# Kernel tuning notes

Hardware: AMD Instinct MI355X
Metric: run time of the kernel (lower is better)

Reference implementation:

```python
import jax, jax.numpy as jnp
import numpy as np

# dims: batch, samples, agents, obs_dim, action_dim, hidden
B, S, N, D, A, H = 512, 64, 8, 64, 16, 256
IN_DIM = (D + A) * N  # 640


def mish(x):
    return x * jnp.tanh(jax.nn.softplus(x))


def setup_inputs() -> dict:
    key = jax.random.key(0)
    ks = jax.random.split(key, 9)
    u = lambda k, shape, fan_in: jax.random.uniform(
        k, shape, jnp.float32, -1.0 / np.sqrt(fan_in), 1.0 / np.sqrt(fan_in))
    return {
        "state": jax.random.normal(ks[0], (B, N, D), jnp.float32),
        "action": jax.random.normal(ks[1], (B, N, A), jnp.float32),
        "W1": u(ks[2], (IN_DIM, H), IN_DIM),
        "b1": u(ks[3], (H,), IN_DIM),
        "W2": u(ks[4], (H, H), H),
        "b2": u(ks[5], (H,), H),
        "W3": u(ks[6], (H, 1), H),
        "b3": u(ks[7], (1,), H),
        # random grand-coalition permutations of the N agents, per (batch, sample)
        "perm": jnp.argsort(jax.random.uniform(ks[8], (B, S, N)), axis=-1).astype(jnp.int32),
    }


def reference(state, action, W1, b1, W2, b2, W3, b3, perm):
    # subcoalition mask [B,S,N,N]: torch builds one-hot(perm) @ tril(ones),
    # i.e. mask[b,s,i,j] = 1 iff j <= perm[b,s,i]
    subcoal = (jnp.arange(N) <= perm[..., None]).astype(state.dtype)
    # gathered actions in coalition order [B,S,N,A]: act_g[b,s,j] = action[b, perm[b,s,j]]
    act_g = action[jnp.arange(B)[:, None, None], perm]
    # masked subcoalition actions [B,S,N,N,A] -> [B,S,N,N*A]
    act = (act_g[:, :, None, :, :] * subcoal[..., None]).reshape(B, S, N, N * A)
    # flattened global obs broadcast over (sample, agent) axes [B,S,N,N*D]
    obs = jnp.broadcast_to(state.reshape(B, 1, 1, N * D), (B, S, N, N * D))
    x = jnp.concatenate([obs, act], axis=-1)  # [B,S,N,IN_DIM]
    # per-agent loop in torch uses shared q1 weights -> single batched MLP
    h = mish(x @ W1 + b1)
    h = mish(h @ W2 + b2)
    q = h @ W3 + b3                   # [B,S,N,1]
    q1 = q.mean(axis=1).squeeze(-1)   # mean over samples -> [B,N]
    return (q1, q1)
```

## Files before the change

kernel.cpp:

```cpp
#include <hip/hip_runtime.h>
#include <hip/hip_bf16.h>

typedef unsigned short ushort_t;
typedef _Float16 half_t;
typedef __attribute__((ext_vector_type(2))) _Float16 half2_t;
typedef __attribute__((ext_vector_type(8))) _Float16 half8_t;
typedef __attribute__((ext_vector_type(2))) float fx2;
typedef __attribute__((ext_vector_type(4))) float floatx4;

#define LOG2E 1.4426950408889634f
#define LN2   0.6931471805599453f

__device__ __forceinline__ float exp2_(float x) {
#if __has_builtin(__builtin_amdgcn_exp2f)
    return __builtin_amdgcn_exp2f(x);
#else
    return exp2f(x);
#endif
}

__device__ __forceinline__ half2_t cvt_pk_f16(float a, float b) {
    auto r = __builtin_amdgcn_cvt_pkrtz(a, b);
    return __builtin_bit_cast(half2_t, r);
}

__device__ __forceinline__ fx2 mish2(fx2 t0) {
    fx2 one = {1.0f, 1.0f};
    fx2 m2  = {-2.0f, -2.0f};
    fx2 u   = {exp2_(t0.x), exp2_(t0.y)};
    fx2 s   = u + one;
    fx2 wv  = __builtin_elementwise_fma(s, s, one);
    fx2 rr  = {__builtin_amdgcn_rcpf(wv.x), __builtin_amdgcn_rcpf(wv.y)};
    fx2 v   = __builtin_elementwise_fma(rr, m2, one);
    return t0 * v;
}

__device__ __forceinline__ float dpp_sum16(float v) {
    int x = __float_as_int(v);
    v += __int_as_float(__builtin_amdgcn_update_dpp(0, x, 0xB1, 0xF, 0xF, true));
    x = __float_as_int(v);
    v += __int_as_float(__builtin_amdgcn_update_dpp(0, x, 0x4E, 0xF, 0xF, true));
    x = __float_as_int(v);
    v += __int_as_float(__builtin_amdgcn_update_dpp(0, x, 0x124, 0xF, 0xF, true));
    x = __float_as_int(v);
    v += __int_as_float(__builtin_amdgcn_update_dpp(0, x, 0x128, 0xF, 0xF, true));
    return v;
}

__global__ __launch_bounds__(256) void prep_kernel(
        const float* __restrict__ state,
        const float* __restrict__ action,
        const float* __restrict__ W1,
        const float* __restrict__ b1,
        const float* __restrict__ W2,
        float* __restrict__ obsW,
        half_t* __restrict__ actW,
        half_t* __restrict__ W2T,
        float* __restrict__ out) {
    int bid = blockIdx.x;
    int t = threadIdx.x;
    if (bid < 512) {
        int b = bid;
        const float* stp = state + (size_t)b * 512;
        const float* w1p = W1 + t;
        float a0 = 0.f, a1 = 0.f, a2 = 0.f, a3 = 0.f;
#pragma unroll 8
        for (int f = 0; f < 512; f += 4) {
            a0 = fmaf(stp[f + 0], w1p[(f + 0) * 256], a0);
            a1 = fmaf(stp[f + 1], w1p[(f + 1) * 256], a1);
            a2 = fmaf(stp[f + 2], w1p[(f + 2) * 256], a2);
            a3 = fmaf(stp[f + 3], w1p[(f + 3) * 256], a3);
        }
        obsW[b * 256 + t] = ((a0 + a1) + (a2 + a3) + b1[t]) * LOG2E;
    } else if (bid < 2560) {
        int idx = bid - 512;
        int j = idx & 7;
        int b0 = (idx >> 3) * 2;
        const float* W1a = W1 + (size_t)(512 + j * 16) * 256;
        float wv[16];
#pragma unroll
        for (int a = 0; a < 16; ++a) wv[a] = W1a[a * 256 + t];
#pragma unroll
        for (int bb = 0; bb < 2; ++bb) {
            int b = b0 + bb;
            const float* acp = action + (size_t)b * 128;
            float acc[8];
#pragma unroll
            for (int n = 0; n < 8; ++n) acc[n] = 0.f;
#pragma unroll
            for (int a = 0; a < 16; ++a) {
#pragma unroll
                for (int n = 0; n < 8; ++n)
                    acc[n] = fmaf(acp[n * 16 + a], wv[a], acc[n]);
            }
#pragma unroll
            for (int n = 0; n < 8; ++n)
                actW[(((size_t)b * 8 + n) * 8 + j) * 256 + t] = (half_t)(acc[n] * LOG2E);
        }
    } else {
        int blk = bid - 2560;
        if (blk < 16) {
            out[blk * 512 + t] = 0.0f;
            out[blk * 512 + 256 + t] = 0.0f;
        }
        int n = blk * 8 + (t >> 5);
        int klo = t & 31;
#pragma unroll
        for (int kk = 0; kk < 8; ++kk) {
            int k = kk * 32 + klo;
            W2T[n * 256 + k] = (half_t)W2[k * 256 + n];
        }
    }
}

#define CHUNK_US 528

__global__ __launch_bounds__(512, 4) void main_kernel(
        const float* __restrict__ obsW, const half_t* __restrict__ actW,
        const half_t* __restrict__ W2T, const int* __restrict__ perm,
        const float* __restrict__ b2,
        const float* __restrict__ W3, const float* __restrict__ b3,
        float* __restrict__ out) {
    __shared__ __align__(16) ushort_t h1[32 * CHUNK_US];
    __shared__ __align__(16) float obsb[256];
    __shared__ int perm_s[64];
    __shared__ float qpart[8][64];
    __shared__ float qv_s[64];

    int t = threadIdx.x;
    int bid = blockIdx.x;
    int b = (bid & 7) * 64 + ((bid >> 3) & 63);
    int sg = bid >> 9;
    int s0 = sg * 8;

    int w = t >> 6;
    int L = t & 63;
    int lo = L & 15;
    int q = L >> 4;

    if (t < 256) obsb[t] = obsW[b * 256 + t];
    else if (t < 320) perm_s[t - 256] = perm[((size_t)b * 64 + s0) * 8 + (t - 256)];

    const half_t* w2base = W2T + ((size_t)(w * 32 + lo)) * 256 + q * 8;
    half8_t bpre[4];
    bpre[0] = *reinterpret_cast<const half8_t*>(w2base + 0 * 16 * 256 + 0 * 32);
    bpre[1] = *reinterpret_cast<const half8_t*>(w2base + 1 * 16 * 256 + 0 * 32);
    bpre[2] = *reinterpret_cast<const half8_t*>(w2base + 0 * 16 * 256 + 1 * 32);
    bpre[3] = *reinterpret_cast<const half8_t*>(w2base + 1 * 16 * 256 + 1 * 32);

    __syncthreads();

    {
        int sl = w;
        int hg = L;
        int g = hg >> 1;
        int ks = g >> 2;
        int qq = g & 3;
        int half = hg & 1;
        const half_t* actg = actW + (size_t)b * 64 * 256 + hg * 4;
        uint2 av[8];
#pragma unroll
        for (int j = 0; j < 8; ++j) {
            int p = perm_s[sl * 8 + j];
            av[j] = *reinterpret_cast<const uint2*>(actg + (p * 8 + j) * 256);
        }
        float4 ob = *reinterpret_cast<const float4*>(obsb + hg * 4);
        fx2 r01 = {ob.x, ob.y};
        fx2 r23 = {ob.z, ob.w};
        ushort_t* dst0 = h1 + (qq * 16) * 8 + half * 4 + ks * CHUNK_US;
#pragma unroll
        for (int j = 0; j < 8; ++j) {
            half2_t a0 = __builtin_bit_cast(half2_t, av[j].x);
            half2_t a1 = __builtin_bit_cast(half2_t, av[j].y);
            r01 += (fx2){(float)a0.x, (float)a0.y};
            r23 += (fx2){(float)a1.x, (float)a1.y};
            fx2 h01 = mish2(r01);
            fx2 h23 = mish2(r23);
            half2_t p0 = cvt_pk_f16(h01.x, h01.y);
            half2_t p1 = cvt_pk_f16(h23.x, h23.y);
            int row = sl * 8 + j;
            int mt = row >> 4, lr = row & 15;
            uint2 pk = make_uint2(__builtin_bit_cast(unsigned, p0),
                                  __builtin_bit_cast(unsigned, p1));
            *reinterpret_cast<uint2*>(dst0 + mt * 8 * CHUNK_US + lr * 8) = pk;
        }
    }
    __syncthreads();

    floatx4 acc[4][2];
#pragma unroll
    for (int mt = 0; mt < 4; ++mt)
#pragma unroll
        for (int nt = 0; nt < 2; ++nt)
            acc[mt][nt] = (floatx4){0.f, 0.f, 0.f, 0.f};

    const ushort_t* h1b = h1 + L * 8;

#pragma unroll
    for (int ks = 0; ks < 8; ++ks) {
        half8_t afr[4];
#pragma unroll
        for (int mt = 0; mt < 4; ++mt)
            afr[mt] = *reinterpret_cast<const half8_t*>(h1b + (mt * 8 + ks) * CHUNK_US);
#pragma unroll
        for (int nt = 0; nt < 2; ++nt) {
            half8_t bfr;
            if (ks == 0)      bfr = bpre[nt];
            else if (ks == 1) bfr = bpre[2 + nt];
            else              bfr = *reinterpret_cast<const half8_t*>(w2base + nt * 16 * 256 + ks * 32);
#pragma unroll
            for (int mt = 0; mt < 4; ++mt)
                acc[mt][nt] = __builtin_amdgcn_mfma_f32_16x16x32_f16(afr[mt], bfr, acc[mt][nt], 0, 0, 0);
        }
    }

    int col0 = w * 32 + 0 * 16 + lo;
    int col1 = w * 32 + 1 * 16 + lo;
    fx2 b2p = {b2[col0] * LOG2E, b2[col1] * LOG2E};
    half2_t w3p = cvt_pk_f16(W3[col0] * LN2, W3[col1] * LN2);
#pragma unroll
    for (int mt = 0; mt < 4; ++mt) {
        float part[4];
#pragma unroll
        for (int r = 0; r < 4; ++r) {
            fx2 t2 = {acc[mt][0][r], acc[mt][1][r]};
            t2 += b2p;
            fx2 h = mish2(t2);
            half2_t hh = cvt_pk_f16(h.x, h.y);
#if __has_builtin(__builtin_amdgcn_fdot2)
            part[r] = __builtin_amdgcn_fdot2(__builtin_bit_cast(__fp16 __attribute__((ext_vector_type(2))), hh),
                                             __builtin_bit_cast(__fp16 __attribute__((ext_vector_type(2))), w3p),
                                             0.0f, false);
#else
            part[r] = (float)hh.x * (float)w3p.x + (float)hh.y * (float)w3p.y;
#endif
        }
#pragma unroll
        for (int r = 0; r < 4; ++r) {
            float v = dpp_sum16(part[r]);
            if (lo == 0) qpart[w][mt * 16 + q * 4 + r] = v;
        }
    }
    __syncthreads();
    if (t < 64) {
        float qv = b3[0];
#pragma unroll
        for (int ww = 0; ww < 8; ++ww) qv += qpart[ww][t];
        qv_s[t] = qv;
    }
    __syncthreads();
    if (t < 8) {
        float p = 0.f;
#pragma unroll
        for (int sl = 0; sl < 8; ++sl)
            p += qv_s[sl * 8 + perm_s[sl * 8 + t]];
        p *= (1.0f / 64.0f);
        atomicAdd(&out[b * 8 + t], p);
        atomicAdd(&out[4096 + b * 8 + t], p);
    }
}

extern "C" void kernel_launch(void* const* d_in, const int* in_sizes, int n_in,
                              void* d_out, int out_size, void* d_ws, size_t ws_size,
                              hipStream_t stream) {
    const float* state  = (const float*)d_in[0];
    const float* action = (const float*)d_in[1];
    const float* W1     = (const float*)d_in[2];
    const float* b1     = (const float*)d_in[3];
    const float* W2     = (const float*)d_in[4];
    const float* b2     = (const float*)d_in[5];
    const float* W3     = (const float*)d_in[6];
    const float* b3     = (const float*)d_in[7];
    const int*   perm   = (const int*)d_in[8];
    float* out = (float*)d_out;

    char* ws = (char*)d_ws;
    float*  obsW = (float*)ws;
    half_t* actW = (half_t*)(ws + 524288);
    half_t* W2T  = (half_t*)(ws + 524288 + 16777216);

    prep_kernel<<<2592, 256, 0, stream>>>(state, action, W1, b1, W2, obsW, actW, W2T, out);
    main_kernel<<<4096, 512, 0, stream>>>(obsW, actW, W2T, perm, b2, W3, b3, out);
}
```

Before: 178.3 us.

## Process two sample groups per block with software-pipelined layer1/MFMA/epilogue overlap

Each block now handles 16 samples (two groups of 8) instead of 8, halving the grid to 2048 blocks. Layer-1 mish for the second group is interleaved with the layer-2 MFMA loop of the first group, and the first group's layer-3 epilogue is interleaved with the second group's MFMA loop. The aim is to hide transcendental and VALU work behind matrix ops and to amortize the per-block setup, the obs load and the W2 prefetch over more samples. In exchange it doubles LDS for h1 to about 67KB and raises register pressure from two accumulator sets, which may reduce occupancy under launch_bounds(512,4).

```diff
diff --git a/kernel.cpp b/kernel.cpp
--- a/kernel.cpp
+++ b/kernel.cpp
@@ -1,10 +1,10 @@
 #include <hip/hip_runtime.h>
-#include <hip/hip_bf16.h>
 
 typedef unsigned short ushort_t;
 typedef _Float16 half_t;
 typedef __attribute__((ext_vector_type(2))) _Float16 half2_t;
 typedef __attribute__((ext_vector_type(8))) _Float16 half8_t;
+typedef __attribute__((ext_vector_type(2))) __fp16 fp16x2;
 typedef __attribute__((ext_vector_type(2))) float fx2;
 typedef __attribute__((ext_vector_type(4))) float floatx4;
 
@@ -22,6 +22,15 @@
 __device__ __forceinline__ half2_t cvt_pk_f16(float a, float b) {
     auto r = __builtin_amdgcn_cvt_pkrtz(a, b);
     return __builtin_bit_cast(half2_t, r);
+}
+
+__device__ __forceinline__ float fdot2_(half2_t a, half2_t b) {
+#if __has_builtin(__builtin_amdgcn_fdot2)
+    return __builtin_amdgcn_fdot2(__builtin_bit_cast(fp16x2, a),
+                                  __builtin_bit_cast(fp16x2, b), 0.0f, false);
+#else
+    return (float)a.x * (float)b.x + (float)a.y * (float)b.y;
+#endif
 }
 
 __device__ __forceinline__ fx2 mish2(fx2 t0) {
@@ -121,17 +130,16 @@
         const float* __restrict__ b2,
         const float* __restrict__ W3, const float* __restrict__ b3,
         float* __restrict__ out) {
-    __shared__ __align__(16) ushort_t h1[32 * CHUNK_US];
+    __shared__ __align__(16) ushort_t h1[2][32 * CHUNK_US];
     __shared__ __align__(16) float obsb[256];
-    __shared__ int perm_s[64];
-    __shared__ float qpart[8][64];
-    __shared__ float qv_s[64];
+    __shared__ int perm_s[128];
+    __shared__ float qpart[2][8][64];
 
     int t = threadIdx.x;
     int bid = blockIdx.x;
     int b = (bid & 7) * 64 + ((bid >> 3) & 63);
-    int sg = bid >> 9;
-    int s0 = sg * 8;
+    int sgp = bid >> 9;
+    int s0 = sgp * 16;
 
     int w = t >> 6;
     int L = t & 63;
@@ -139,35 +147,36 @@
     int q = L >> 4;
 
     if (t < 256) obsb[t] = obsW[b * 256 + t];
-    else if (t < 320) perm_s[t - 256] = perm[((size_t)b * 64 + s0) * 8 + (t - 256)];
+    else if (t < 384) perm_s[t - 256] = perm[((size_t)b * 64 + s0) * 8 + (t - 256)];
 
     const half_t* w2base = W2T + ((size_t)(w * 32 + lo)) * 256 + q * 8;
     half8_t bpre[4];
-    bpre[0] = *reinterpret_cast<const half8_t*>(w2base + 0 * 16 * 256 + 0 * 32);
-    bpre[1] = *reinterpret_cast<const half8_t*>(w2base + 1 * 16 * 256 + 0 * 32);
-    bpre[2] = *reinterpret_cast<const half8_t*>(w2base + 0 * 16 * 256 + 1 * 32);
-    bpre[3] = *reinterpret_cast<const half8_t*>(w2base + 1 * 16 * 256 + 1 * 32);
+    bpre[0] = *reinterpret_cast<const half8_t*>(w2base + 0 * 4096 + 0 * 32);
+    bpre[1] = *reinterpret_cast<const half8_t*>(w2base + 1 * 4096 + 0 * 32);
+    bpre[2] = *reinterpret_cast<const half8_t*>(w2base + 0 * 4096 + 1 * 32);
+    bpre[3] = *reinterpret_cast<const half8_t*>(w2base + 1 * 4096 + 1 * 32);
+
+    int g = L >> 1;
+    int ksg = g >> 2;
+    int qq = g & 3;
+    int halfsel = L & 1;
+    const half_t* actg = actW + (size_t)b * 64 * 256 + L * 4;
+    int dstoff = qq * 128 + halfsel * 4 + ksg * CHUNK_US;
 
     __syncthreads();
 
+    float4 ob = *reinterpret_cast<const float4*>(obsb + L * 4);
+
     {
-        int sl = w;
-        int hg = L;
-        int g = hg >> 1;
-        int ks = g >> 2;
-        int qq = g & 3;
-        int half = hg & 1;
-        const half_t* actg = actW + (size_t)b * 64 * 256 + hg * 4;
         uint2 av[8];
 #pragma unroll
         for (int j = 0; j < 8; ++j) {
-            int p = perm_s[sl * 8 + j];
+            int p = perm_s[(0 * 8 + w) * 8 + j];
             av[j] = *reinterpret_cast<const uint2*>(actg + (p * 8 + j) * 256);
         }
-        float4 ob = *reinterpret_cast<const float4*>(obsb + hg * 4);
         fx2 r01 = {ob.x, ob.y};
         fx2 r23 = {ob.z, ob.w};
-        ushort_t* dst0 = h1 + (qq * 16) * 8 + half * 4 + ks * CHUNK_US;
+        ushort_t* dst0 = h1[0] + dstoff;
 #pragma unroll
         for (int j = 0; j < 8; ++j) {
             half2_t a0 = __builtin_bit_cast(half2_t, av[j].x);
@@ -176,87 +185,130 @@
             r23 += (fx2){(float)a1.x, (float)a1.y};
             fx2 h01 = mish2(r01);
             fx2 h23 = mish2(r23);
-            half2_t p0 = cvt_pk_f16(h01.x, h01.y);
-            half2_t p1 = cvt_pk_f16(h23.x, h23.y);
-            int row = sl * 8 + j;
-            int mt = row >> 4, lr = row & 15;
-            uint2 pk = make_uint2(__builtin_bit_cast(unsigned, p0),
-                                  __builtin_bit_cast(unsigned, p1));
-            *reinterpret_cast<uint2*>(dst0 + mt * 8 * CHUNK_US + lr * 8) = pk;
+            int row = w * 8 + j;
+            int mt2 = row >> 4, lr = row & 15;
+            uint2 pk = make_uint2(__builtin_bit_cast(unsigned, cvt_pk_f16(h01.x, h01.y)),
+                                  __builtin_bit_cast(unsigned, cvt_pk_f16(h23.x, h23.y)));
+            *reinterpret_cast<uint2*>(dst0 + mt2 * 8 * CHUNK_US + lr * 8) = pk;
         }
     }
     __syncthreads();
 
-    floatx4 acc[4][2];
+    floatx4 acc0[4][2];
 #pragma unroll
     for (int mt = 0; mt < 4; ++mt)
 #pragma unroll
-        for (int nt = 0; nt < 2; ++nt)
-            acc[mt][nt] = (floatx4){0.f, 0.f, 0.f, 0.f};
-
-    const ushort_t* h1b = h1 + L * 8;
-
-#pragma unroll
-    for (int ks = 0; ks < 8; ++ks) {
-        half8_t afr[4];
-#pragma unroll
-        for (int mt = 0; mt < 4; ++mt)
-            afr[mt] = *reinterpret_cast<const half8_t*>(h1b + (mt * 8 + ks) * CHUNK_US);
-#pragma unroll
-        for (int nt = 0; nt < 2; ++nt) {
-            half8_t bfr;
-            if (ks == 0)      bfr = bpre[nt];
-            else if (ks == 1) bfr = bpre[2 + nt];
-            else              bfr = *reinterpret_cast<const half8_t*>(w2base + nt * 16 * 256 + ks * 32);
+        for (int nt = 0; nt < 2; ++nt) acc0[mt][nt] = (floatx4){0.f, 0.f, 0.f, 0.f};
+    {
+        uint2 av[8];
+#pragma unroll
+        for (int j = 0; j < 8; ++j) {
+            int p = perm_s[(1 * 8 + w) * 8 + j];
+            av[j] = *reinterpret_cast<const uint2*>(actg + (p * 8 + j) * 256);
+        }
+        fx2 r01 = {ob.x, ob.y};
+        fx2 r23 = {ob.z, ob.w};
+        ushort_t* dst1 = h1[1] + dstoff;
+        const ushort_t* h1b0 = h1[0] + L * 8;
+#pragma unroll
+        for (int ks = 0; ks < 8; ++ks) {
+            half8_t afr[4];
 #pragma unroll
             for (int mt = 0; mt < 4; ++mt)
-                acc[mt][nt] = __builtin_amdgcn_mfma_f32_16x16x32_f16(afr[mt], bfr, acc[mt][nt], 0, 0, 0);
-        }
-    }
+                afr[mt] = *reinterpret_cast<const half8_t*>(h1b0 + (mt * 8 + ks) * CHUNK_US);
+            half8_t bfr0 = (ks == 0) ? bpre[0] : (ks == 1) ? bpre[2]
+                         : *reinterpret_cast<const half8_t*>(w2base + 0 * 4096 + ks * 32);
+            half8_t bfr1 = (ks == 0) ? bpre[1] : (ks == 1) ? bpre[3]
+                         : *reinterpret_cast<const half8_t*>(w2base + 1 * 4096 + ks * 32);
+#pragma unroll
+            for (int mt = 0; mt < 4; ++mt) {
+                acc0[mt][0] = __builtin_amdgcn_mfma_f32_16x16x32_f16(afr[mt], bfr0, acc0[mt][0], 0, 0, 0);
+                acc0[mt][1] = __builtin_amdgcn_mfma_f32_16x16x32_f16(afr[mt], bfr1, acc0[mt][1], 0, 0, 0);
+            }
+            {
+                half2_t a0 = __builtin_bit_cast(half2_t, av[ks].x);
+                half2_t a1 = __builtin_bit_cast(half2_t, av[ks].y);
+                r01 += (fx2){(float)a0.x, (float)a0.y};
+                r23 += (fx2){(float)a1.x, (float)a1.y};
+                fx2 h01 = mish2(r01);
+                fx2 h23 = mish2(r23);
+                int row = w * 8 + ks;
+                int mt2 = row >> 4, lr = row & 15;
+                uint2 pk = make_uint2(__builtin_bit_cast(unsigned, cvt_pk_f16(h01.x, h01.y)),
+                                      __builtin_bit_cast(unsigned, cvt_pk_f16(h23.x, h23.y)));
+                *reinterpret_cast<uint2*>(dst1 + mt2 * 8 * CHUNK_US + lr * 8) = pk;
+            }
+        }
+    }
+    __syncthreads();
 
     int col0 = w * 32 + 0 * 16 + lo;
     int col1 = w * 32 + 1 * 16 + lo;
     fx2 b2p = {b2[col0] * LOG2E, b2[col1] * LOG2E};
     half2_t w3p = cvt_pk_f16(W3[col0] * LN2, W3[col1] * LN2);
-#pragma unroll
-    for (int mt = 0; mt < 4; ++mt) {
-        float part[4];
-#pragma unroll
-        for (int r = 0; r < 4; ++r) {
-            fx2 t2 = {acc[mt][0][r], acc[mt][1][r]};
-            t2 += b2p;
-            fx2 h = mish2(t2);
-            half2_t hh = cvt_pk_f16(h.x, h.y);
-#if __has_builtin(__builtin_amdgcn_fdot2)
-            part[r] = __builtin_amdgcn_fdot2(__builtin_bit_cast(__fp16 __attribute__((ext_vector_type(2))), hh),
-                                             __builtin_bit_cast(__fp16 __attribute__((ext_vector_type(2))), w3p),
-                                             0.0f, false);
-#else
-            part[r] = (float)hh.x * (float)w3p.x + (float)hh.y * (float)w3p.y;
-#endif
-        }
-#pragma unroll
-        for (int r = 0; r < 4; ++r) {
-            float v = dpp_sum16(part[r]);
-            if (lo == 0) qpart[w][mt * 16 + q * 4 + r] = v;
-        }
+
+    floatx4 acc1[4][2];
+#pragma unroll
+    for (int mt = 0; mt < 4; ++mt)
+#pragma unroll
+        for (int nt = 0; nt < 2; ++nt) acc1[mt][nt] = (floatx4){0.f, 0.f, 0.f, 0.f};
+    {
+        const ushort_t* h1b1 = h1[1] + L * 8;
+#pragma unroll
+        for (int ks = 0; ks < 8; ++ks) {
+            half8_t afr[4];
+#pragma unroll
+            for (int mt = 0; mt < 4; ++mt)
+                afr[mt] = *reinterpret_cast<const half8_t*>(h1b1 + (mt * 8 + ks) * CHUNK_US);
+            half8_t bfr0 = (ks == 0) ? bpre[0] : (ks == 1) ? bpre[2]
+                         : *reinterpret_cast<const half8_t*>(w2base + 0 * 4096 + ks * 32);
+            half8_t bfr1 = (ks == 0) ? bpre[1] : (ks == 1) ? bpre[3]
+                         : *reinterpret_cast<const half8_t*>(w2base + 1 * 4096 + ks * 32);
+#pragma unroll
+            for (int mt = 0; mt < 4; ++mt) {
+                acc1[mt][0] = __builtin_amdgcn_mfma_f32_16x16x32_f16(afr[mt], bfr0, acc1[mt][0], 0, 0, 0);
+                acc1[mt][1] = __builtin_amdgcn_mfma_f32_16x16x32_f16(afr[mt], bfr1, acc1[mt][1], 0, 0, 0);
+            }
+#pragma unroll
+            for (int v = 0; v < 2; ++v) {
+                int idx = ks * 2 + v;
+                int mt = idx >> 2, r = idx & 3;
+                fx2 t2 = {acc0[mt][0][r], acc0[mt][1][r]};
+                t2 += b2p;
+                fx2 hh = mish2(t2);
+                float part = fdot2_(cvt_pk_f16(hh.x, hh.y), w3p);
+                float s = dpp_sum16(part);
+                if (lo == 0) qpart[0][w][mt * 16 + q * 4 + r] = s;
+            }
+        }
+    }
+#pragma unroll
+    for (int idx = 0; idx < 16; ++idx) {
+        int mt = idx >> 2, r = idx & 3;
+        fx2 t2 = {acc1[mt][0][r], acc1[mt][1][r]};
+        t2 += b2p;
+        fx2 hh = mish2(t2);
+        float part = fdot2_(cvt_pk_f16(hh.x, hh.y), w3p);
+        float s = dpp_sum16(part);
+        if (lo == 0) qpart[1][w][mt * 16 + q * 4 + r] = s;
     }
     __syncthreads();
-    if (t < 64) {
-        float qv = b3[0];
-#pragma unroll
-        for (int ww = 0; ww < 8; ++ww) qv += qpart[ww][t];
-        qv_s[t] = qv;
-    }
-    __syncthreads();
-    if (t < 8) {
+
+    if (t < 16) {
+        int h = t >> 3, i = t & 7;
         float p = 0.f;
 #pragma unroll
-        for (int sl = 0; sl < 8; ++sl)
-            p += qv_s[sl * 8 + perm_s[sl * 8 + t]];
+        for (int sl = 0; sl < 8; ++sl) {
+            int k = perm_s[(h * 8 + sl) * 8 + i];
+            int row = sl * 8 + k;
+            float qv = b3[0];
+#pragma unroll
+            for (int ww = 0; ww < 8; ++ww) qv += qpart[h][ww][row];
+            p += qv;
+        }
         p *= (1.0f / 64.0f);
-        atomicAdd(&out[b * 8 + t], p);
-        atomicAdd(&out[4096 + b * 8 + t], p);
+        atomicAdd(&out[b * 8 + i], p);
+        atomicAdd(&out[4096 + b * 8 + i], p);
     }
 }
 
@@ -280,5 +332,5 @@
     half_t* W2T  = (half_t*)(ws + 524288 + 16777216);
 
     prep_kernel<<<2592, 256, 0, stream>>>(state, action, W1, b1, W2, obsW, actW, W2T, out);
-    main_kernel<<<4096, 512, 0, stream>>>(obsW, actW, W2T, perm, b2, W3, b3, out);
-}
+    main_kernel<<<2048, 512, 0, stream>>>(obsW, actW, W2T, perm, b2, W3, b3, out);
+}
```

Result: faster. 165.3 us (-7.3%).
